# Kernel optimization log

Measured on AMD Instinct MI355X. Metric: run time of the kernel, lower is better.

## Reference

```python
import jax, jax.numpy as jnp
import numpy as np

DT = 0.001
HIDDEN = 512
OUT = 128

def setup_inputs() -> dict:
    key = jax.random.key(0)
    k1, k2 = jax.random.split(key)
    x = jax.random.normal(k1, (64, 2048, HIDDEN), dtype=jnp.float32)
    # torch Linear default init ~ U(-1/sqrt(fan_in), 1/sqrt(fan_in)), weight shape [out, in]
    lim = 1.0 / np.sqrt(HIDDEN)
    W = jax.random.uniform(k2, (OUT, HIDDEN), dtype=jnp.float32, minval=-lim, maxval=lim)
    tau_syn = jnp.asarray(0.5, dtype=jnp.float32)  # tau_syn_out (used as tau_syn_inv)
    tau_mem = jnp.asarray(0.5, dtype=jnp.float32)  # tau_mem_out (used as tau_mem_inv)
    return {"x": x, "W": W, "tau_syn": tau_syn, "tau_mem": tau_mem}

def reference(x, W, tau_syn, tau_mem):
    # SNNDecode.forward: clamp taus, permute to [seq, batch, in], per-step
    # Linear + norse LI (leaky integrator) feed-forward step with v_leak = 0.
    tau_syn = jnp.clip(tau_syn, 0.0, 1.0)
    tau_mem = jnp.clip(tau_mem, 0.0, 1.0)
    batch, seq, _ = x.shape
    # The per-step Linear is recurrence-independent: hoist it into one big GEMM.
    # z_all: [seq, batch, out]
    z_all = jnp.einsum('bsh,oh->sbo', x, W)
    v0 = jnp.zeros((batch, OUT), dtype=x.dtype)
    i0 = jnp.zeros((batch, OUT), dtype=x.dtype)

    def step(carry, z):
        v, i = carry
        # li_feed_forward_step: dv = dt*tau_mem_inv*((v_leak - v) + i)
        v_new = v + DT * tau_mem * (i - v)
        i_dec = i - DT * tau_syn * i
        i_new = i_dec + z
        return (v_new, i_new), v_new

    (v_f, i_f), voltages = jax.lax.scan(step, (v0, i0), z_all)
    # output stacked over time: [seq, batch, out]; final state (v, i)
    return voltages, v_f, i_f
```

## Files before the change

### kernel.cpp

```cpp
#include <hip/hip_runtime.h>
#include <hip/hip_bf16.h>


typedef __attribute__((ext_vector_type(4))) float    f4;
typedef __attribute__((ext_vector_type(8))) short    s8;
typedef __attribute__((ext_vector_type(4))) unsigned u4;

#define SEQ    2048
#define HID    512
#define CHAINS 8192
#define VOLT   16777216
#define NCH    32

__device__ __forceinline__ float clamp01(float x) { return fminf(fmaxf(x, 0.f), 1.f); }

__device__ __forceinline__ unsigned pkbf(float x, float y) {
  float2 t; t.x = x; t.y = y;
  union { __hip_bfloat162 h; unsigned u; } c;
  c.h = __float22bfloat162_rn(t);
  return c.u;
}

__device__ __forceinline__ short f2bf(float f) {
  union { float f; unsigned u; } c; c.f = f;
  unsigned u = c.u;
  unsigned r = (u + 0x7fffu + ((u >> 16) & 1u)) >> 16;
  return (short)r;
}

__device__ __forceinline__ int swz(int row, int k) {
  return (row * 64 + k) ^ ((row & 7) << 3);
}

__global__ __launch_bounds__(256) void k_wconv(const float* __restrict__ W,
                                               unsigned short* __restrict__ Wb) {
  const int i = blockIdx.x * 256 + threadIdx.x;
  const f4 lo = ((const f4*)W)[2 * i];
  const f4 hi = ((const f4*)W)[2 * i + 1];
  s8 v;
#pragma unroll
  for (int j = 0; j < 4; ++j) { v[j] = f2bf(lo[j]); v[j + 4] = f2bf(hi[j]); }
  ((s8*)Wb)[i] = v;
}

__global__ __launch_bounds__(256, 2) void k_gemm(const float* __restrict__ X,
                                                 const unsigned short* __restrict__ Wb,
                                                 float* __restrict__ Z,
                                                 const float* __restrict__ tau_syn,
                                                 const float* __restrict__ tau_mem,
                                                 float* __restrict__ ws) {
  __shared__ __align__(16) char smem[65536];
  short* const AS = (short*)smem;
  short* const BS = (short*)(smem + 32768);
  float* const ZS = (float*)smem;

  const int tid = threadIdx.x;
  const int blk = blockIdx.x;
  const int m0  = blk << 7;
  const int bI  = blk >> 4;
  const int t0  = (blk & 15) << 7;

  const int rbase = tid >> 3;
  const int coff  = (tid & 7) << 3;

  const int lane = tid & 63;
  const int wid  = tid >> 6;
  const int wmb  = (wid >> 1) << 6;
  const int wnb  = (wid & 1) << 6;
  const int lr   = lane & 15;
  const int lk   = (lane >> 4) << 3;

  const float* pX[4];
  const unsigned short* pW[4];
#pragma unroll
  for (int c = 0; c < 4; ++c) {
    const int row = (c << 5) + rbase;
    pX[c] = X + (size_t)(m0 + row) * HID + coff;
    pW[c] = Wb + (size_t)row * HID + coff;
  }

  f4 acc[4][4];
#pragma unroll
  for (int mi = 0; mi < 4; ++mi)
#pragma unroll
    for (int ni = 0; ni < 4; ++ni) acc[mi][ni] = (f4){0.f, 0.f, 0.f, 0.f};

  f4 xa[2][4][2];
  s8 wv[2][4];
#pragma unroll
  for (int c = 0; c < 4; ++c) {
    xa[0][c][0] = *(const f4*)(pX[c]);
    xa[0][c][1] = *(const f4*)(pX[c] + 4);
    wv[0][c]    = *(const s8*)(pW[c]);
  }

#pragma unroll
  for (int ks = 0; ks < 8; ++ks) {
    const int cur = ks & 1;
    short* const Ac = AS + (cur << 13);
    short* const Bc = BS + (cur << 13);
#pragma unroll
    for (int c = 0; c < 4; ++c) {
      const int row = (c << 5) + rbase;
      u4 va;
      va[0] = pkbf(xa[cur][c][0][0], xa[cur][c][0][1]);
      va[1] = pkbf(xa[cur][c][0][2], xa[cur][c][0][3]);
      va[2] = pkbf(xa[cur][c][1][0], xa[cur][c][1][1]);
      va[3] = pkbf(xa[cur][c][1][2], xa[cur][c][1][3]);
      *(u4*)&Ac[swz(row, coff)] = va;
      *(s8*)&Bc[swz(row, coff)] = wv[cur][c];
    }
    __syncthreads();
    if (ks < 7) {
      const int k0 = (ks + 1) << 6;
#pragma unroll
      for (int c = 0; c < 4; ++c) {
        xa[cur ^ 1][c][0] = *(const f4*)(pX[c] + k0);
        xa[cur ^ 1][c][1] = *(const f4*)(pX[c] + k0 + 4);
        wv[cur ^ 1][c]    = *(const s8*)(pW[c] + k0);
      }
    }
#pragma unroll
    for (int kk = 0; kk < 2; ++kk) {
      s8 af[4], bg[4];
#pragma unroll
      for (int mi = 0; mi < 4; ++mi)
        af[mi] = *(const s8*)&Ac[swz(wmb + (mi << 4) + lr, (kk << 5) + lk)];
#pragma unroll
      for (int ni = 0; ni < 4; ++ni)
        bg[ni] = *(const s8*)&Bc[swz(wnb + (ni << 4) + lr, (kk << 5) + lk)];
#pragma unroll
      for (int mi = 0; mi < 4; ++mi)
#pragma unroll
        for (int ni = 0; ni < 4; ++ni)
          acc[mi][ni] = __builtin_amdgcn_mfma_f32_16x16x32_bf16(af[mi], bg[ni],
                                                                acc[mi][ni], 0, 0, 0);
    }
  }

  __syncthreads();
  const int rr = (lane >> 4) << 2;
#pragma unroll
  for (int mi = 0; mi < 4; ++mi)
#pragma unroll
    for (int ni = 0; ni < 4; ++ni)
#pragma unroll
      for (int r = 0; r < 4; ++r)
        ZS[(wmb + (mi << 4) + rr + r) * 128 + wnb + (ni << 4) + lr] = acc[mi][ni][r];
  __syncthreads();

  {
    float* const Zrow = Z + (size_t)t0 * 8192 + (bI << 7);
#pragma unroll
    for (int i = 0; i < 16; ++i) {
      const int idx  = (i << 8) + tid;
      const int toff = idx >> 5;
      const int c4   = idx & 31;
      *(f4*)(Zrow + (size_t)toff * 8192 + (c4 << 2)) = *(const f4*)&ZS[toff * 128 + (c4 << 2)];
    }
  }
  {
    const float a  = 0.001f * clamp01(tau_mem[0]);
    const float eb = 1.f - 0.001f * clamp01(tau_syn[0]);
    const int h = tid >> 7, col = tid & 127;
    const float* zs = ZS + ((h << 6) * 128) + col;
    float v = 0.f, ii = 0.f;
#pragma unroll 8
    for (int j = 0; j < 64; ++j) {
      const float z = zs[j * 128];
      v  = v + a * (ii - v);
      ii = eb * ii + z;
    }
    const int q     = ((blk & 15) << 1) + h;
    const int chain = (bI << 7) + col;
    ws[q * CHAINS + chain]                 = v;
    ws[NCH * CHAINS + q * CHAINS + chain]  = ii;
  }
}

__global__ __launch_bounds__(256) void k_combine(const float* __restrict__ tau_syn,
                                                 const float* __restrict__ tau_mem,
                                                 float* __restrict__ Out,
                                                 float* __restrict__ ws) {
  const int c = blockIdx.x * 256 + threadIdx.x;
  const float a  = 0.001f * clamp01(tau_mem[0]);
  const float bb = 0.001f * clamp01(tau_syn[0]);
  const float ea = 1.f - a, eb = 1.f - bb;
  float P = 1.f, Q = 0.f, R = 1.f;
#pragma unroll
  for (int j = 0; j < 64; ++j) { float Pn = P * ea; Q = P * a + Q * eb; P = Pn; R *= eb; }
  float* vend = ws;
  float* iend = ws + NCH * CHAINS;
  float sv = 0.f, si = 0.f;
  for (int q = 0; q < NCH; ++q) {
    const int idx = q * CHAINS + c;
    const float ve = vend[idx], ie = iend[idx];
    vend[idx] = sv;  iend[idx] = si;
    const float nv = P * sv + Q * si + ve;
    si = R * si + ie;
    sv = nv;
  }
  Out[VOLT + c] = sv;
  Out[VOLT + CHAINS + c] = si;
}

__global__ __launch_bounds__(256) void k_emit(const float* __restrict__ tau_syn,
                                              const float* __restrict__ tau_mem,
                                              float* Z,
                                              const float* __restrict__ ws) {
  const int tid = threadIdx.x;
  const int cg = (blockIdx.x & 31) * 64 + (tid & 63);
  const int q  = (blockIdx.x >> 5) * 4 + (tid >> 6);
  const float a  = 0.001f * clamp01(tau_mem[0]);
  const float eb = 1.f - 0.001f * clamp01(tau_syn[0]);
  f4* z4 = (f4*)Z;
  const f4* vin = (const f4*)ws;
  const f4* iin = vin + NCH * 2048;
  f4 v  = vin[q * 2048 + cg];
  f4 ii = iin[q * 2048 + cg];
  const int tb = q << 6;
#pragma unroll 8
  for (int j = 0; j < 64; ++j) {
    const size_t idx = (size_t)(tb + j) * 2048 + cg;
    f4 z = z4[idx];
    v  = v + a * (ii - v);
    z4[idx] = v;
    ii = eb * ii + z;
  }
}

extern "C" void kernel_launch(void* const* d_in, const int* in_sizes, int n_in,
                              void* d_out, int out_size, void* d_ws, size_t ws_size,
                              hipStream_t stream) {
  const float* X   = (const float*)d_in[0];
  const float* W   = (const float*)d_in[1];
  const float* tsy = (const float*)d_in[2];
  const float* tme = (const float*)d_in[3];
  float* Out = (float*)d_out;
  float* ws  = (float*)d_ws;
  unsigned short* Wb = (unsigned short*)((char*)d_ws + (2u << 20));

  k_wconv<<<32, 256, 0, stream>>>(W, Wb);
  k_gemm<<<1024, 256, 0, stream>>>(X, Wb, Out, tsy, tme, ws);
  k_combine<<<32, 256, 0, stream>>>(tsy, tme, Out, ws);
  k_emit<<<256, 256, 0, stream>>>(tsy, tme, Out, ws);
}
```

Baseline: 113.7 us.

## Load GEMM B fragments directly from global, triple-buffer X, widen emit grid

The GEMM kernel now reads W bf16 fragments straight from global memory (L2-resident) into registers instead of staging them through shared memory. This removes the B-tile LDS writes and reads. X prefetch goes from double to triple buffering, two k-steps ahead. The emit kernel switches from float4 to float2 per thread and doubles its grid for more parallelism. In exchange the GEMM uses more registers, which may lower occupancy, and issues more global loads per wave.

```diff
diff --git a/kernel.cpp b/kernel.cpp
--- a/kernel.cpp
+++ b/kernel.cpp
@@ -3,6 +3,7 @@
 
 
 typedef __attribute__((ext_vector_type(4))) float    f4;
+typedef __attribute__((ext_vector_type(2))) float    f2;
 typedef __attribute__((ext_vector_type(8))) short    s8;
 typedef __attribute__((ext_vector_type(4))) unsigned u4;
 
@@ -51,7 +52,6 @@
                                                  float* __restrict__ ws) {
   __shared__ __align__(16) char smem[65536];
   short* const AS = (short*)smem;
-  short* const BS = (short*)(smem + 32768);
   float* const ZS = (float*)smem;
 
   const int tid = threadIdx.x;
@@ -71,13 +71,13 @@
   const int lk   = (lane >> 4) << 3;
 
   const float* pX[4];
-  const unsigned short* pW[4];
-#pragma unroll
-  for (int c = 0; c < 4; ++c) {
-    const int row = (c << 5) + rbase;
-    pX[c] = X + (size_t)(m0 + row) * HID + coff;
-    pW[c] = Wb + (size_t)row * HID + coff;
-  }
+#pragma unroll
+  for (int c = 0; c < 4; ++c)
+    pX[c] = X + (size_t)(m0 + (c << 5) + rbase) * HID + coff;
+  const unsigned short* pB[4];
+#pragma unroll
+  for (int ni = 0; ni < 4; ++ni)
+    pB[ni] = Wb + (size_t)(wnb + (ni << 4) + lr) * HID + lk;
 
   f4 acc[4][4];
 #pragma unroll
@@ -85,20 +85,19 @@
 #pragma unroll
     for (int ni = 0; ni < 4; ++ni) acc[mi][ni] = (f4){0.f, 0.f, 0.f, 0.f};
 
-  f4 xa[2][4][2];
-  s8 wv[2][4];
+  f4 xa[3][4][2];
 #pragma unroll
   for (int c = 0; c < 4; ++c) {
     xa[0][c][0] = *(const f4*)(pX[c]);
     xa[0][c][1] = *(const f4*)(pX[c] + 4);
-    wv[0][c]    = *(const s8*)(pW[c]);
+    xa[1][c][0] = *(const f4*)(pX[c] + 64);
+    xa[1][c][1] = *(const f4*)(pX[c] + 68);
   }
 
 #pragma unroll
   for (int ks = 0; ks < 8; ++ks) {
-    const int cur = ks & 1;
-    short* const Ac = AS + (cur << 13);
-    short* const Bc = BS + (cur << 13);
+    const int cur = ks % 3;
+    short* const Ac = AS + ((ks & 1) << 13);
 #pragma unroll
     for (int c = 0; c < 4; ++c) {
       const int row = (c << 5) + rbase;
@@ -108,32 +107,34 @@
       va[2] = pkbf(xa[cur][c][1][0], xa[cur][c][1][1]);
       va[3] = pkbf(xa[cur][c][1][2], xa[cur][c][1][3]);
       *(u4*)&Ac[swz(row, coff)] = va;
-      *(s8*)&Bc[swz(row, coff)] = wv[cur][c];
     }
     __syncthreads();
-    if (ks < 7) {
-      const int k0 = (ks + 1) << 6;
+    s8 bg[2][4];
+#pragma unroll
+    for (int kk = 0; kk < 2; ++kk)
+#pragma unroll
+      for (int ni = 0; ni < 4; ++ni)
+        bg[kk][ni] = *(const s8*)(pB[ni] + (ks << 6) + (kk << 5));
+    if (ks < 6) {
+      const int k0 = (ks + 2) << 6;
+      const int nxt = (ks + 2) % 3;
 #pragma unroll
       for (int c = 0; c < 4; ++c) {
-        xa[cur ^ 1][c][0] = *(const f4*)(pX[c] + k0);
-        xa[cur ^ 1][c][1] = *(const f4*)(pX[c] + k0 + 4);
-        wv[cur ^ 1][c]    = *(const s8*)(pW[c] + k0);
+        xa[nxt][c][0] = *(const f4*)(pX[c] + k0);
+        xa[nxt][c][1] = *(const f4*)(pX[c] + k0 + 4);
       }
     }
 #pragma unroll
     for (int kk = 0; kk < 2; ++kk) {
-      s8 af[4], bg[4];
+      s8 af[4];
 #pragma unroll
       for (int mi = 0; mi < 4; ++mi)
         af[mi] = *(const s8*)&Ac[swz(wmb + (mi << 4) + lr, (kk << 5) + lk)];
 #pragma unroll
-      for (int ni = 0; ni < 4; ++ni)
-        bg[ni] = *(const s8*)&Bc[swz(wnb + (ni << 4) + lr, (kk << 5) + lk)];
-#pragma unroll
       for (int mi = 0; mi < 4; ++mi)
 #pragma unroll
         for (int ni = 0; ni < 4; ++ni)
-          acc[mi][ni] = __builtin_amdgcn_mfma_f32_16x16x32_bf16(af[mi], bg[ni],
+          acc[mi][ni] = __builtin_amdgcn_mfma_f32_16x16x32_bf16(af[mi], bg[kk][ni],
                                                                 acc[mi][ni], 0, 0, 0);
     }
   }
@@ -209,22 +210,22 @@
                                               float* Z,
                                               const float* __restrict__ ws) {
   const int tid = threadIdx.x;
-  const int cg = (blockIdx.x & 31) * 64 + (tid & 63);
-  const int q  = (blockIdx.x >> 5) * 4 + (tid >> 6);
+  const int cg = (blockIdx.x & 63) * 64 + (tid & 63);
+  const int q  = (blockIdx.x >> 6) * 4 + (tid >> 6);
   const float a  = 0.001f * clamp01(tau_mem[0]);
   const float eb = 1.f - 0.001f * clamp01(tau_syn[0]);
-  f4* z4 = (f4*)Z;
-  const f4* vin = (const f4*)ws;
-  const f4* iin = vin + NCH * 2048;
-  f4 v  = vin[q * 2048 + cg];
-  f4 ii = iin[q * 2048 + cg];
+  f2* z2 = (f2*)Z;
+  const f2* vin = (const f2*)ws;
+  const f2* iin = vin + NCH * 4096;
+  f2 v  = vin[q * 4096 + cg];
+  f2 ii = iin[q * 4096 + cg];
   const int tb = q << 6;
 #pragma unroll 8
   for (int j = 0; j < 64; ++j) {
-    const size_t idx = (size_t)(tb + j) * 2048 + cg;
-    f4 z = z4[idx];
+    const size_t idx = (size_t)(tb + j) * 4096 + cg;
+    f2 z = z2[idx];
     v  = v + a * (ii - v);
-    z4[idx] = v;
+    z2[idx] = v;
     ii = eb * ii + z;
   }
 }
@@ -243,5 +244,5 @@
   k_wconv<<<32, 256, 0, stream>>>(W, Wb);
   k_gemm<<<1024, 256, 0, stream>>>(X, Wb, Out, tsy, tme, ws);
   k_combine<<<32, 256, 0, stream>>>(tsy, tme, Out, ws);
-  k_emit<<<256, 256, 0, stream>>>(tsy, tme, Out, ws);
-}
+  k_emit<<<512, 256, 0, stream>>>(tsy, tme, Out, ws);
+}
```

Measured after the change: 104.6 us. 7.9% less time.
